# Performance work log

Measured on AMD Instinct MI355X. Metric: run time of the kernel, lower is better.

The kernel has to match this reference:

```python
import jax, jax.numpy as jnp
import numpy as np

D_MODEL = 768
N_HEADS = 12
D_HEAD = D_MODEL // N_HEADS


def setup_inputs() -> dict:
    key = jax.random.key(0)
    k_x, k_qw, k_qb, k_ow, k_ob = jax.random.split(key, 5)
    B, N = 2, 4096
    scale = 1.0 / np.sqrt(D_MODEL)
    return {
        "x": jax.random.normal(k_x, (B, N, D_MODEL), dtype=jnp.float32),
        # torch nn.Linear stores weight as [out_features, in_features]
        "qkv_w": jax.random.uniform(k_qw, (3 * D_MODEL, D_MODEL), jnp.float32, -scale, scale),
        "qkv_b": jax.random.uniform(k_qb, (3 * D_MODEL,), jnp.float32, -scale, scale),
        "out_w": jax.random.uniform(k_ow, (D_MODEL, D_MODEL), jnp.float32, -scale, scale),
        "out_b": jax.random.uniform(k_ob, (D_MODEL,), jnp.float32, -scale, scale),
    }


def reference(x, qkv_w, qkv_b, out_w, out_b):
    B, N, D = x.shape
    qkv = x @ qkv_w.T + qkv_b                                   # [B, N, 3D]
    qkv = qkv.reshape(B, N, 3, N_HEADS, D_HEAD)
    qkv = jnp.transpose(qkv, (2, 0, 3, 1, 4))                    # [3, B, H, N, d]
    q, k, v = qkv[0], qkv[1], qkv[2]
    scores = jnp.einsum("bhqd,bhkd->bhqk", q, k) / np.sqrt(D_HEAD)
    attn = jax.nn.softmax(scores, axis=-1)
    out = jnp.einsum("bhqk,bhkd->bhqd", attn, v)                 # [B, H, N, d]
    out = jnp.transpose(out, (0, 2, 1, 3)).reshape(B, N, D)
    return out @ out_w.T + out_b
```

## Files before the change

### kernel.cpp

```cpp
#include <hip/hip_runtime.h>
#include <cstdint>

#define SEQ 4096
#define NH 12
#define DH 64
#define DM 768
#define MT 8192
#define QKVN 2304

typedef __bf16 bf16;
typedef __attribute__((ext_vector_type(8))) __bf16 bf16x8;
typedef __attribute__((ext_vector_type(4))) __bf16 bf16x4;
typedef __attribute__((ext_vector_type(2))) __bf16 bf16x2;
typedef __attribute__((ext_vector_type(4))) float f32x4;
typedef __attribute__((ext_vector_type(16))) float f32x16;
typedef __attribute__((ext_vector_type(2))) int int2v;

__device__ __forceinline__ void async_ld16(const void* g, void* lds) {
  __builtin_amdgcn_global_load_lds(
      (__attribute__((address_space(1))) void*)(void*)g,
      (__attribute__((address_space(3))) void*)lds, 16, 0, 0);
}

__device__ __forceinline__ int pexp2_pair(float s0, float s1) {
  int j0 = (int)__builtin_fmaf(s0, 128.0f, 16251.5f);
  int j1 = (int)__builtin_fmaf(s1, 128.0f, 16251.5f);
  return j0 | (j1 << 16);
}

__device__ __forceinline__ void lane32_swap(int& a, int& b) {
#if __has_builtin(__builtin_amdgcn_permlane32_swap)
  int2v r = __builtin_amdgcn_permlane32_swap(a, b, false, false);
  a = r.x; b = r.y;
#else
  int hi = (threadIdx.x & 63) >> 5;
  int ra = __shfl_xor(a, 32, 64), rb = __shfl_xor(b, 32, 64);
  int na = hi ? rb : a;
  int nb = hi ? b : ra;
  a = na; b = nb;
#endif
}

#define NX4  (MT * DM / 4)
#define NW14 (QKVN * DM / 4)
#define NW24 (DM * DM / 4)
__global__ void cvt_all(const float* __restrict__ x, const float* __restrict__ w1,
                        const float* __restrict__ w2, bf16* __restrict__ xb,
                        bf16* __restrict__ wb1, bf16* __restrict__ wb2) {
  int i = blockIdx.x * blockDim.x + threadIdx.x;
  const float* src; bf16* dst; int j;
  if (i < NX4) { src = x; dst = xb; j = i; }
  else if (i < NX4 + NW14) { src = w1; dst = wb1; j = i - NX4; }
  else if (i < NX4 + NW14 + NW24) { src = w2; dst = wb2; j = i - NX4 - NW14; }
  else return;
  f32x4 v = ((const f32x4*)src)[j];
  bf16x4 o;
  o.x = (bf16)v.x; o.y = (bf16)v.y; o.z = (bf16)v.z; o.w = (bf16)v.w;
  ((bf16x4*)dst)[j] = o;
}

template<int MODE>
__global__ __launch_bounds__(256) void gemm_bt(
    const bf16* __restrict__ A, const bf16* __restrict__ Bw,
    const float* __restrict__ bias,
    bf16* __restrict__ outQ, bf16* __restrict__ outK, bf16* __restrict__ outVt,
    float* __restrict__ outF,
    int M, int N, int K)
{
  __shared__ bf16 sA[128 * 32];
  __shared__ bf16 sB[128 * 32];
  __shared__ bf16 sT[MODE == 0 ? 64 * 136 : 1];
  const int tid  = threadIdx.x;
  const int wave = tid >> 6;
  const int lane = tid & 63;
  const int l15  = lane & 15;
  const int quad = lane >> 4;

  constexpr int NT = (MODE == 0) ? (QKVN / 128) : (DM / 128);
  const int lin = blockIdx.x;
  const int rem = lin % (NT * 8);
  const int m0 = ((lin / (NT * 8)) * 8 + (rem % 8)) * 128;
  const int n0 = (rem / 8) * 128;

  const int rowbase = (wave >> 1) * 64;
  const int colbase = (wave & 1) * 64;

  f32x4 acc[4][4] = {};

  const int sr = lane >> 2;
  const int sc = (lane & 3) * 8;

  for (int kt = 0; kt < K; kt += 32) {
#pragma unroll
    for (int p = 0; p < 4; ++p) {
      int chunk = p * 4 + wave;
      int r = (chunk & 7) * 16 + sr;
      if (chunk < 8) {
        async_ld16(A + (size_t)(m0 + r) * K + kt + sc, &sA[(chunk & 7) * 512]);
      } else {
        async_ld16(Bw + (size_t)(n0 + r) * K + kt + sc, &sB[(chunk & 7) * 512]);
      }
    }
    __syncthreads();

    bf16x8 af[4], bfr[4];
#pragma unroll
    for (int rt = 0; rt < 4; ++rt)
      af[rt] = *(const bf16x8*)&sA[(rowbase + rt * 16 + l15) * 32 + quad * 8];
#pragma unroll
    for (int ct = 0; ct < 4; ++ct)
      bfr[ct] = *(const bf16x8*)&sB[(colbase + ct * 16 + l15) * 32 + quad * 8];
#pragma unroll
    for (int rt = 0; rt < 4; ++rt)
#pragma unroll
      for (int ct = 0; ct < 4; ++ct)
        acc[rt][ct] = __builtin_amdgcn_mfma_f32_16x16x32_bf16(af[rt], bfr[ct], acc[rt][ct], 0, 0, 0);
    __syncthreads();
  }

  if (MODE == 0) {
    const int g = n0 / DM;
    if (g < 2) {
      const float qscale = 0.125f * 1.4426950408889634f;
#pragma unroll
      for (int ct = 0; ct < 4; ++ct) {
        int j = n0 + colbase + ct * 16 + l15;
        float bj = bias[j];
        int f = j % DM;
        int h = f >> 6, d = f & 63;
#pragma unroll
        for (int rt = 0; rt < 4; ++rt) {
          int mrow = m0 + rowbase + rt * 16 + quad * 4;
#pragma unroll
          for (int r = 0; r < 4; ++r) {
            float v = acc[rt][ct][r] + bj;
            int m = mrow + r;
            int b = m >> 12, n = m & 4095;
            int bh = b * NH + h;
            if (g == 0) outQ[((size_t)bh * SEQ + n) * DH + d] = (bf16)(v * qscale);
            else        outK[((size_t)bh * SEQ + n) * DH + d] = (bf16)v;
          }
        }
      }
    } else {
      const int f0 = n0 - 2 * DM;
      const int b = m0 >> 12, n0m = m0 & 4095;
#pragma unroll
      for (int p = 0; p < 2; ++p) {
        __syncthreads();
        if (colbase == p * 64) {
#pragma unroll
          for (int ct = 0; ct < 4; ++ct) {
            int jl = ct * 16 + l15;
            float bj = bias[n0 + p * 64 + jl];
#pragma unroll
            for (int rt = 0; rt < 4; ++rt) {
              int ml = rowbase + rt * 16 + quad * 4;
#pragma unroll
              for (int r = 0; r < 4; ++r)
                sT[jl * 136 + ml + r] = (bf16)(acc[rt][ct][r] + bj);
            }
          }
        }
        __syncthreads();
#pragma unroll
        for (int p2 = 0; p2 < 4; ++p2) {
          int slot = p2 * 256 + tid;
          int jr = slot >> 4, mc = (slot & 15) * 8;
          int fj = f0 + p * 64 + jr;
          int h = fj >> 6, d = fj & 63;
          *(bf16x8*)&outVt[((size_t)(b * NH + h) * DH + d) * SEQ + n0m + mc] =
              *(const bf16x8*)&sT[jr * 136 + mc];
        }
      }
    }
  } else {
#pragma unroll
    for (int ct = 0; ct < 4; ++ct) {
      int j = n0 + colbase + ct * 16 + l15;
      float bj = bias[j];
#pragma unroll
      for (int rt = 0; rt < 4; ++rt) {
        int mrow = m0 + rowbase + rt * 16 + quad * 4;
#pragma unroll
        for (int r = 0; r < 4; ++r)
          outF[(size_t)(mrow + r) * N + j] = acc[rt][ct][r] + bj;
      }
    }
  }
}

__global__ __launch_bounds__(256) void flash_attn(
    const bf16* __restrict__ Q, const bf16* __restrict__ Kg,
    const bf16* __restrict__ Vt, bf16* __restrict__ Oout)
{
  __shared__ bf16 sK[2][64 * 64];
  __shared__ bf16 sV[2][64 * 64];

  const int tid  = threadIdx.x;
  const int wave = tid >> 6;
  const int lane = tid & 63;
  const int l31  = lane & 31;
  const int hi   = lane >> 5;
  const int bh = blockIdx.y;
  const int q0w = blockIdx.x * 128 + wave * 32;

  const bf16* Qb = Q  + (size_t)bh * SEQ * DH;
  const bf16* Kb = Kg + (size_t)bh * SEQ * DH;
  const bf16* Vb = Vt + (size_t)bh * DH * SEQ;

  const int srow = lane >> 3;
  const int spg  = lane & 7;

  bf16x8 qf[4];
#pragma unroll
  for (int dc = 0; dc < 4; ++dc)
    qf[dc] = *(const bf16x8*)&Qb[(size_t)(q0w + l31) * DH + dc * 16 + hi * 8];

  bf16x8 ones1;
#pragma unroll
  for (int j = 0; j < 8; ++j) ones1[j] = (bf16)1.0f;

  f32x16 o0 = {}, o1 = {}, o2 = {};
  f32x16 zc = {};

  const int keyk = (l31 & 7) ^ (((l31 >> 3) & 3) << 1);
  int kOff[4], vOff[4];
#pragma unroll
  for (int dc = 0; dc < 4; ++dc)
    kOff[dc] = l31 * 64 + (((dc * 2 + hi) ^ keyk) * 8);
#pragma unroll
  for (int k4 = 0; k4 < 4; ++k4)
    vOff[k4] = l31 * 64 + (((k4 * 2 + hi) ^ keyk) * 8);

  auto stage = [&](int kt, int buf) {
#pragma unroll
    for (int j = 0; j < 2; ++j) {
      int r0 = wave * 16 + j * 8;
      int row = r0 + srow;
      int lg = spg ^ (row & 7) ^ (((row >> 3) & 3) << 1);
      async_ld16(Kb + (size_t)(kt + row) * DH + lg * 8, &sK[buf][r0 * 64]);
      async_ld16(Vb + (size_t)row * SEQ + kt + lg * 8, &sV[buf][r0 * 64]);
    }
  };

  auto compute = [&](const bf16* sKp, const bf16* sVp) {
#pragma unroll
    for (int kb = 0; kb < 2; ++kb) {
      f32x16 s;
      {
        bf16x8 kf = *(const bf16x8*)&sKp[kOff[0] + kb * 2048];
        s = __builtin_amdgcn_mfma_f32_32x32x16_bf16(kf, qf[0], zc, 0, 0, 0);
      }
#pragma unroll
      for (int dc = 1; dc < 4; ++dc) {
        bf16x8 kf = *(const bf16x8*)&sKp[kOff[dc] + kb * 2048];
        s = __builtin_amdgcn_mfma_f32_32x32x16_bf16(kf, qf[dc], s, 0, 0, 0);
      }
#pragma unroll
      for (int kc = 0; kc < 2; ++kc) {
        int g0a = pexp2_pair(s[8 * kc + 0], s[8 * kc + 1]);
        int g0b = pexp2_pair(s[8 * kc + 2], s[8 * kc + 3]);
        int g1a = pexp2_pair(s[8 * kc + 4], s[8 * kc + 5]);
        int g1b = pexp2_pair(s[8 * kc + 6], s[8 * kc + 7]);
        lane32_swap(g0a, g1a);
        lane32_swap(g0b, g1b);
        union { int i[4]; bf16x8 v; } Af;
        Af.i[0] = g0a; Af.i[1] = g0b; Af.i[2] = g1a; Af.i[3] = g1b;
        bf16x8 vf0 = *(const bf16x8*)&sVp[vOff[kb * 2 + kc]];
        bf16x8 vf1 = *(const bf16x8*)&sVp[vOff[kb * 2 + kc] + 2048];
        o0 = __builtin_amdgcn_mfma_f32_32x32x16_bf16(Af.v, vf0, o0, 0, 0, 0);
        o1 = __builtin_amdgcn_mfma_f32_32x32x16_bf16(Af.v, vf1, o1, 0, 0, 0);
        o2 = __builtin_amdgcn_mfma_f32_32x32x16_bf16(Af.v, ones1, o2, 0, 0, 0);
      }
    }
  };

  stage(0, 0);
  __syncthreads();

  for (int kt = 0; kt < SEQ; kt += 128) {
    if (kt + 64 < SEQ) stage(kt + 64, 1);
    compute(sK[0], sV[0]);
    __syncthreads();
    if (kt + 128 < SEQ) stage(kt + 128, 0);
    compute(sK[1], sV[1]);
    __syncthreads();
  }

  const int bg = bh / NH, h = bh % NH;
#pragma unroll
  for (int i = 0; i < 16; ++i) {
    int ql = 8 * (i >> 2) + (i & 3) + 4 * hi;
    float inv = 1.0f / o2[i];
    size_t base = (size_t)(bg * SEQ + q0w + ql) * DM + h * DH;
    Oout[base + l31]      = (bf16)(o0[i] * inv);
    Oout[base + 32 + l31] = (bf16)(o1[i] * inv);
  }
}

extern "C" void kernel_launch(void* const* d_in, const int* in_sizes, int n_in,
                              void* d_out, int out_size, void* d_ws, size_t ws_size,
                              hipStream_t stream) {
  const float* x     = (const float*)d_in[0];
  const float* qkv_w = (const float*)d_in[1];
  const float* qkv_b = (const float*)d_in[2];
  const float* out_w = (const float*)d_in[3];
  const float* out_b = (const float*)d_in[4];
  float* out = (float*)d_out;

  char* w = (char*)d_ws;
  bf16* xb    = (bf16*)w; w += (size_t)MT * DM * 2;
  bf16* wqkv  = (bf16*)w; w += (size_t)QKVN * DM * 2;
  bf16* wout  = (bf16*)w; w += (size_t)DM * DM * 2;
  bf16* Qw    = (bf16*)w; w += (size_t)MT * DM * 2;
  bf16* Kw    = (bf16*)w; w += (size_t)MT * DM * 2;
  bf16* Vtw   = (bf16*)w; w += (size_t)MT * DM * 2;
  bf16* attnV = (bf16*)w; w += (size_t)MT * DM * 2;

  const int tot4 = NX4 + NW14 + NW24;
  cvt_all<<<dim3((tot4 + 255) / 256), 256, 0, stream>>>(x, qkv_w, out_w, xb, wqkv, wout);

  gemm_bt<0><<<dim3((QKVN / 128) * (MT / 128)), 256, 0, stream>>>(
      xb, wqkv, qkv_b, Qw, Kw, Vtw, nullptr, MT, QKVN, DM);

  flash_attn<<<dim3(SEQ / 128, 2 * NH), 256, 0, stream>>>(Qw, Kw, Vtw, attnV);

  gemm_bt<1><<<dim3((DM / 128) * (MT / 128)), 256, 0, stream>>>(
      attnV, wout, out_b, nullptr, nullptr, nullptr, out, MT, DM, DM);
}
```

Before: 282.5 us.

## Fuse fp32-to-bf16 conversion of x and out_w into GEMM tile loads

Removes the separate conversion pass over the activation x and the output projection weight. The GEMMs now async-load fp32 tiles into LDS with an XOR swizzle and pack them to bf16 in registers before the MFMA. This drops a full read and write of x in bf16 and one launch's worth of work. In exchange, the fp32 operand uses twice the LDS traffic and space per tile, and conversion instructions are added to the inner loop. Each A tile is also converted repeatedly, once per N-tile block.

```diff
diff --git a/kernel.cpp b/kernel.cpp
--- a/kernel.cpp
+++ b/kernel.cpp
@@ -20,6 +20,18 @@
   __builtin_amdgcn_global_load_lds(
       (__attribute__((address_space(1))) void*)(void*)g,
       (__attribute__((address_space(3))) void*)lds, 16, 0, 0);
+}
+
+__device__ __forceinline__ int pk_bf16(float a, float b) {
+#if __has_builtin(__builtin_amdgcn_cvt_pk_bf16_f32)
+  union { bf16x2 v; int i; } u;
+  u.v = __builtin_amdgcn_cvt_pk_bf16_f32(a, b);
+  return u.i;
+#else
+  union { int i; bf16 h[2]; } u;
+  u.h[0] = (bf16)a; u.h[1] = (bf16)b;
+  return u.i;
+#endif
 }
 
 __device__ __forceinline__ int pexp2_pair(float s0, float s1) {
@@ -41,35 +53,29 @@
 #endif
 }
 
-#define NX4  (MT * DM / 4)
-#define NW14 (QKVN * DM / 4)
-#define NW24 (DM * DM / 4)
-__global__ void cvt_all(const float* __restrict__ x, const float* __restrict__ w1,
-                        const float* __restrict__ w2, bf16* __restrict__ xb,
-                        bf16* __restrict__ wb1, bf16* __restrict__ wb2) {
+__global__ void cvt_w(const float* __restrict__ in, bf16* __restrict__ out, int n4) {
   int i = blockIdx.x * blockDim.x + threadIdx.x;
-  const float* src; bf16* dst; int j;
-  if (i < NX4) { src = x; dst = xb; j = i; }
-  else if (i < NX4 + NW14) { src = w1; dst = wb1; j = i - NX4; }
-  else if (i < NX4 + NW14 + NW24) { src = w2; dst = wb2; j = i - NX4 - NW14; }
-  else return;
-  f32x4 v = ((const f32x4*)src)[j];
+  if (i >= n4) return;
+  f32x4 v = ((const f32x4*)in)[i];
   bf16x4 o;
   o.x = (bf16)v.x; o.y = (bf16)v.y; o.z = (bf16)v.z; o.w = (bf16)v.w;
-  ((bf16x4*)dst)[j] = o;
+  ((bf16x4*)out)[i] = o;
 }
 
 template<int MODE>
 __global__ __launch_bounds__(256) void gemm_bt(
-    const bf16* __restrict__ A, const bf16* __restrict__ Bw,
+    const void* __restrict__ Av, const void* __restrict__ Bv,
     const float* __restrict__ bias,
     bf16* __restrict__ outQ, bf16* __restrict__ outK, bf16* __restrict__ outVt,
     float* __restrict__ outF,
     int M, int N, int K)
 {
-  __shared__ bf16 sA[128 * 32];
-  __shared__ bf16 sB[128 * 32];
-  __shared__ bf16 sT[MODE == 0 ? 64 * 136 : 1];
+  __shared__ float sAf[MODE == 0 ? 128 * 32 : 1];
+  __shared__ bf16  sAh[MODE == 0 ? 1 : 128 * 32];
+  __shared__ bf16  sBh[MODE == 0 ? 128 * 32 : 1];
+  __shared__ float sBf[MODE == 0 ? 1 : 128 * 32];
+  __shared__ bf16  sT[MODE == 0 ? 64 * 136 : 1];
+
   const int tid  = threadIdx.x;
   const int wave = tid >> 6;
   const int lane = tid & 63;
@@ -87,29 +93,74 @@
 
   f32x4 acc[4][4] = {};
 
-  const int sr = lane >> 2;
-  const int sc = (lane & 3) * 8;
+  const int sr  = lane >> 2;
+  const int sc  = (lane & 3) * 8;
+  const int fr  = lane >> 3;
+  const int fg  = (lane & 7) ^ (lane >> 3);
+  const int k8  = l15 & 7;
+
+  const float* Afp = (const float*)Av;
+  const bf16*  Ahp = (const bf16*)Av;
+  const bf16*  Bhp = (const bf16*)Bv;
+  const float* Bfp = (const float*)Bv;
 
   for (int kt = 0; kt < K; kt += 32) {
 #pragma unroll
-    for (int p = 0; p < 4; ++p) {
+    for (int p = 0; p < 6; ++p) {
       int chunk = p * 4 + wave;
-      int r = (chunk & 7) * 16 + sr;
-      if (chunk < 8) {
-        async_ld16(A + (size_t)(m0 + r) * K + kt + sc, &sA[(chunk & 7) * 512]);
+      if (MODE == 0) {
+        if (chunk < 16) {
+          int row = chunk * 8 + fr;
+          async_ld16(Afp + (size_t)(m0 + row) * K + kt + fg * 4, &sAf[chunk * 256]);
+        } else {
+          int bc = chunk - 16;
+          int r = bc * 16 + sr;
+          async_ld16(Bhp + (size_t)(n0 + r) * K + kt + sc, &sBh[bc * 512]);
+        }
       } else {
-        async_ld16(Bw + (size_t)(n0 + r) * K + kt + sc, &sB[(chunk & 7) * 512]);
+        if (chunk < 8) {
+          int r = chunk * 16 + sr;
+          async_ld16(Ahp + (size_t)(m0 + r) * K + kt + sc, &sAh[chunk * 512]);
+        } else {
+          int bc = chunk - 8;
+          int row = bc * 8 + fr;
+          async_ld16(Bfp + (size_t)(n0 + row) * K + kt + fg * 4, &sBf[bc * 256]);
+        }
       }
     }
     __syncthreads();
 
     bf16x8 af[4], bfr[4];
 #pragma unroll
-    for (int rt = 0; rt < 4; ++rt)
-      af[rt] = *(const bf16x8*)&sA[(rowbase + rt * 16 + l15) * 32 + quad * 8];
-#pragma unroll
-    for (int ct = 0; ct < 4; ++ct)
-      bfr[ct] = *(const bf16x8*)&sB[(colbase + ct * 16 + l15) * 32 + quad * 8];
+    for (int rt = 0; rt < 4; ++rt) {
+      int r = rowbase + rt * 16 + l15;
+      if (MODE == 0) {
+        int pg0 = (quad * 2) ^ k8, pg1 = (quad * 2 + 1) ^ k8;
+        f32x4 a0 = *(const f32x4*)&sAf[r * 32 + pg0 * 4];
+        f32x4 a1 = *(const f32x4*)&sAf[r * 32 + pg1 * 4];
+        union { int i[4]; bf16x8 v; } u;
+        u.i[0] = pk_bf16(a0.x, a0.y); u.i[1] = pk_bf16(a0.z, a0.w);
+        u.i[2] = pk_bf16(a1.x, a1.y); u.i[3] = pk_bf16(a1.z, a1.w);
+        af[rt] = u.v;
+      } else {
+        af[rt] = *(const bf16x8*)&sAh[r * 32 + quad * 8];
+      }
+    }
+#pragma unroll
+    for (int ct = 0; ct < 4; ++ct) {
+      int r = colbase + ct * 16 + l15;
+      if (MODE == 0) {
+        bfr[ct] = *(const bf16x8*)&sBh[r * 32 + quad * 8];
+      } else {
+        int pg0 = (quad * 2) ^ k8, pg1 = (quad * 2 + 1) ^ k8;
+        f32x4 b0 = *(const f32x4*)&sBf[r * 32 + pg0 * 4];
+        f32x4 b1 = *(const f32x4*)&sBf[r * 32 + pg1 * 4];
+        union { int i[4]; bf16x8 v; } u;
+        u.i[0] = pk_bf16(b0.x, b0.y); u.i[1] = pk_bf16(b0.z, b0.w);
+        u.i[2] = pk_bf16(b1.x, b1.y); u.i[3] = pk_bf16(b1.z, b1.w);
+        bfr[ct] = u.v;
+      }
+    }
 #pragma unroll
     for (int rt = 0; rt < 4; ++rt)
 #pragma unroll
@@ -310,22 +361,20 @@
   float* out = (float*)d_out;
 
   char* w = (char*)d_ws;
-  bf16* xb    = (bf16*)w; w += (size_t)MT * DM * 2;
   bf16* wqkv  = (bf16*)w; w += (size_t)QKVN * DM * 2;
-  bf16* wout  = (bf16*)w; w += (size_t)DM * DM * 2;
   bf16* Qw    = (bf16*)w; w += (size_t)MT * DM * 2;
   bf16* Kw    = (bf16*)w; w += (size_t)MT * DM * 2;
   bf16* Vtw   = (bf16*)w; w += (size_t)MT * DM * 2;
   bf16* attnV = (bf16*)w; w += (size_t)MT * DM * 2;
 
-  const int tot4 = NX4 + NW14 + NW24;
-  cvt_all<<<dim3((tot4 + 255) / 256), 256, 0, stream>>>(x, qkv_w, out_w, xb, wqkv, wout);
+  const int nw4 = QKVN * DM / 4;
+  cvt_w<<<dim3((nw4 + 255) / 256), 256, 0, stream>>>(qkv_w, wqkv, nw4);
 
   gemm_bt<0><<<dim3((QKVN / 128) * (MT / 128)), 256, 0, stream>>>(
-      xb, wqkv, qkv_b, Qw, Kw, Vtw, nullptr, MT, QKVN, DM);
+      x, wqkv, qkv_b, Qw, Kw, Vtw, nullptr, MT, QKVN, DM);
 
   flash_attn<<<dim3(SEQ / 128, 2 * NH), 256, 0, stream>>>(Qw, Kw, Vtw, attnV);
 
   gemm_bt<1><<<dim3((DM / 128) * (MT / 128)), 256, 0, stream>>>(
-      attnV, wout, out_b, nullptr, nullptr, nullptr, out, MT, DM, DM);
-}
+      attnV, out_w, out_b, nullptr, nullptr, nullptr, out, MT, DM, DM);
+}
```

After: 301.3 us. 6.7% more time.
